# Performance work log

Measured on AMD Instinct MI355X. Metric: run time of the kernel, lower is better.

The kernel has to match this reference:

```python
import jax, jax.numpy as jnp
import numpy as np

N_U = 200000
N_I = 100000
DIM = 128
N_E = 1500000
N_LAYERS = 2


def setup_inputs() -> dict:
    key = jax.random.key(0)
    k1, k2, k3, k4 = jax.random.split(key, 4)
    # xavier-uniform-ish init (bounded values); exact init scheme irrelevant for kernel correctness
    bound = float(np.sqrt(6.0 / (N_U + DIM)))
    u_emb = jax.random.uniform(k1, (N_U, DIM), jnp.float32, -bound, bound)
    bound_i = float(np.sqrt(6.0 / (N_I + DIM)))
    i_emb = jax.random.uniform(k2, (N_I, DIM), jnp.float32, -bound_i, bound_i)
    u_idx = jax.random.randint(k3, (N_E,), 0, N_U, dtype=jnp.int64 if jax.config.jax_enable_x64 else jnp.int32)
    i_idx = jax.random.randint(k4, (N_E,), 0, N_I, dtype=jnp.int64 if jax.config.jax_enable_x64 else jnp.int32)
    return {"u_emb": u_emb, "i_emb": i_emb, "u_idx": u_idx, "i_idx": i_idx}


def _prop(x, r, c, n):
    # symmetric-normalized gather-scale-scatter (SpMM), as in _LightGCN._prop
    deg = jnp.bincount(jnp.concatenate([r, c]), length=n).astype(x.dtype)
    norm = (jnp.clip(deg[r], 1e-10) ** -0.5) * (jnp.clip(deg[c], 1e-10) ** -0.5)  # [2E]
    msg = x[c] * norm[:, None]  # [2E, dim]
    return jax.ops.segment_sum(msg, r, num_segments=n)


def reference(u_emb, i_emb, u_idx, i_idx):
    n_u = u_emb.shape[0]
    n = n_u + i_emb.shape[0]
    it = i_idx + n_u
    r = jnp.concatenate([u_idx, it])  # row (destination) indices
    c = jnp.concatenate([it, u_idx])  # col (source) indices
    x = jnp.concatenate([u_emb, i_emb], axis=0)  # [n, dim]
    outs = [x]
    for _ in range(N_LAYERS):
        x = _prop(x, r, c, n)
        outs.append(x)
    fin = jnp.mean(jnp.stack(outs), axis=0)
    return (fin[:n_u], fin[n_u:])
```

## Files before the change

kernel.cpp:

```cpp
#include <hip/hip_runtime.h>

#define DIM 128
#define NBLK 256
#define BKT_BITS 9
#define BKT_ROWS 512
#define MAXBUK 1024

using f16 = _Float16;
using f16x4 = __attribute__((ext_vector_type(4))) f16;
using f32x4 = __attribute__((ext_vector_type(4))) float;


__device__ __forceinline__ int permb(int b) { return ((b & 7) << 5) | (b >> 3); }

__global__ __launch_bounds__(256) void k_hist(const int* __restrict__ u_idx,
                                              const int* __restrict__ i_idx,
                                              int E, int n_u, int NBUK,
                                              int* __restrict__ hist) {
    __shared__ int h[MAXBUK];
    int b = blockIdx.x, tid = threadIdx.x;
    for (int j = tid; j < NBUK; j += 256) h[j] = 0;
    __syncthreads();
    int chunk = (E + NBLK - 1) / NBLK;
    int i0 = b * chunk, i1 = E < i0 + chunk ? E : i0 + chunk;
    for (int i = i0 + tid; i < i1; i += 256) {
        int u = __builtin_nontemporal_load(&u_idx[i]);
        int t = __builtin_nontemporal_load(&i_idx[i]) + n_u;
        atomicAdd(&h[u >> BKT_BITS], 1);
        atomicAdd(&h[t >> BKT_BITS], 1);
    }
    __syncthreads();
    int pb = permb(b);
    for (int j = tid; j < NBUK; j += 256) hist[j * NBLK + pb] = h[j];
}

__global__ __launch_bounds__(256) void k_scanB(int* __restrict__ hist,
                                               int* __restrict__ bb) {
    __shared__ int sh[256];
    int k = blockIdx.x, t = threadIdx.x;
    int v = hist[k * NBLK + t];
    sh[t] = v;
    __syncthreads();
    for (int off = 1; off < 256; off <<= 1) {
        int tmp = (t >= off) ? sh[t - off] : 0;
        __syncthreads();
        sh[t] += tmp;
        __syncthreads();
    }
    hist[k * NBLK + t] = sh[t] - v;
    if (t == 255) bb[k] = sh[255];
}

__global__ __launch_bounds__(1024) void k_scanT(int* __restrict__ bb, int NBUK) {
    __shared__ int sh[1024];
    int t = threadIdx.x;
    int v = (t < NBUK) ? bb[t] : 0;
    sh[t] = v;
    __syncthreads();
    for (int off = 1; off < 1024; off <<= 1) {
        int tmp = (t >= off) ? sh[t - off] : 0;
        __syncthreads();
        sh[t] += tmp;
        __syncthreads();
    }
    if (t < NBUK) bb[t] = sh[t] - v;
    if (t == NBUK - 1) bb[NBUK] = sh[t];
}

__global__ __launch_bounds__(256) void k_scatter(const int* __restrict__ u_idx,
                                                 const int* __restrict__ i_idx,
                                                 int E, int n_u, int NBUK,
                                                 const int* __restrict__ hist,
                                                 const int* __restrict__ bb,
                                                 unsigned* __restrict__ pre) {
    __shared__ int boff[MAXBUK];
    __shared__ int cnt[MAXBUK];
    int b = blockIdx.x, tid = threadIdx.x;
    int pb = permb(b);
    for (int j = tid; j < NBUK; j += 256) {
        boff[j] = bb[j] + hist[j * NBLK + pb];
        cnt[j] = 0;
    }
    __syncthreads();
    int chunk = (E + NBLK - 1) / NBLK;
    int i0 = b * chunk, i1 = E < i0 + chunk ? E : i0 + chunk;
    for (int i = i0 + tid; i < i1; i += 256) {
        int u = __builtin_nontemporal_load(&u_idx[i]);
        int t = __builtin_nontemporal_load(&i_idx[i]) + n_u;
        int ku = u >> BKT_BITS, kt = t >> BKT_BITS;
        int p1 = atomicAdd(&cnt[ku], 1);
        pre[boff[ku] + p1] = ((unsigned)t << BKT_BITS) | (unsigned)(u & (BKT_ROWS - 1));
        int p2 = atomicAdd(&cnt[kt], 1);
        pre[boff[kt] + p2] = ((unsigned)u << BKT_BITS) | (unsigned)(t & (BKT_ROWS - 1));
    }
}

__global__ __launch_bounds__(256) void k_place(const int* __restrict__ bb, int n, int n_u,
                                               const unsigned* __restrict__ pre,
                                               const float* __restrict__ u_emb,
                                               const float* __restrict__ i_emb,
                                               int* __restrict__ row_ptr,
                                               float* __restrict__ rnorm,
                                               int* __restrict__ adj,
                                               f16* __restrict__ xh0) {
    __shared__ int cnt[BKT_ROWS];
    __shared__ int cur[BKT_ROWS];
    __shared__ int ps[256];
    int b = blockIdx.x, t = threadIdx.x;
    int r0 = b << BKT_BITS;
    int base = bb[b], end = bb[b + 1];
    cnt[t] = 0;
    cnt[t + 256] = 0;
    __syncthreads();
    for (int i = base + t; i < end; i += 256)
        atomicAdd(&cnt[pre[i] & (BKT_ROWS - 1)], 1);
    __syncthreads();
    int a0 = cnt[2 * t], a1 = cnt[2 * t + 1];
    int pv = a0 + a1;
    ps[t] = pv;
    __syncthreads();
    for (int off = 1; off < 256; off <<= 1) {
        int tmp = (t >= off) ? ps[t - off] : 0;
        __syncthreads();
        ps[t] += tmp;
        __syncthreads();
    }
    int ex = ps[t] - pv;
    int e0 = base + ex;
    int e1 = e0 + a0;
    cur[2 * t] = e0;
    cur[2 * t + 1] = e1;
    int rows = n - r0; if (rows > BKT_ROWS) rows = BKT_ROWS;
    if (2 * t < rows) {
        row_ptr[r0 + 2 * t] = e0;
        rnorm[r0 + 2 * t] = (a0 > 0) ? rsqrtf(2.0f * (float)a0) : 0.0f;
    }
    if (2 * t + 1 < rows) {
        row_ptr[r0 + 2 * t + 1] = e1;
        rnorm[r0 + 2 * t + 1] = (a1 > 0) ? rsqrtf(2.0f * (float)a1) : 0.0f;
    }
    if (t == 0 && r0 + BKT_ROWS >= n) row_ptr[n] = end;
    __syncthreads();
    for (int i = base + t; i < end; i += 256) {
        unsigned p = pre[i];
        int rl = (int)(p & (BKT_ROWS - 1));
        int c = (int)(p >> BKT_BITS);
        int pos = atomicAdd(&cur[rl], 1);
        adj[pos] = c;
    }
    for (int g = t; g < rows * 32; g += 256) {
        int vr = g >> 5;
        int lane = g & 31;
        int v = r0 + vr;
        int d = cnt[vr];
        float r = (d > 0) ? rsqrtf(2.0f * (float)d) : 0.0f;
        const float* src = (v < n_u) ? (u_emb + (size_t)v * DIM)
                                     : (i_emb + (size_t)(v - n_u) * DIM);
        f32x4 x = __builtin_nontemporal_load(
            reinterpret_cast<const f32x4*>(src + lane * 4));
        f16x4 o;
        o[0] = (f16)(x[0] * r);
        o[1] = (f16)(x[1] * r);
        o[2] = (f16)(x[2] * r);
        o[3] = (f16)(x[3] * r);
        *reinterpret_cast<f16x4*>(xh0 + (size_t)v * DIM + lane * 4) = o;
    }
}


template <int MODE>
__global__ __launch_bounds__(256) void k_spmm(const int* __restrict__ row_ptr,
                                              const int* __restrict__ adj,
                                              const float* __restrict__ rnorm,
                                              const f16* __restrict__ xh,
                                              const f16* __restrict__ xh0e,
                                              const float* __restrict__ u_emb,
                                              const float* __restrict__ i_emb,
                                              int n_u, int n,
                                              float* __restrict__ y,
                                              f16* __restrict__ yh) {
    int g = blockIdx.x * blockDim.x + threadIdx.x;
    int row = g >> 5;
    int lane = g & 31;
    if (row >= n) return;
    int s = row_ptr[row];
    int e = row_ptr[row + 1];
    float rnr = rnorm[row];
    f32x4 acc = {0.f, 0.f, 0.f, 0.f};
    const f16* xb = xh + lane * 4;
    int e1 = e - 1;
    for (int k = s; k < e; k += 4) {
        int k1 = k + 1, k2 = k + 2, k3 = k + 3;
        int c0 = adj[k];
        int c1 = adj[(k1 <= e1) ? k1 : e1];
        int c2 = adj[(k2 <= e1) ? k2 : e1];
        int c3 = adj[(k3 <= e1) ? k3 : e1];
        float w1 = (k1 < e) ? 1.f : 0.f;
        float w2 = (k2 < e) ? 1.f : 0.f;
        float w3 = (k3 < e) ? 1.f : 0.f;
        f16x4 v0 = *reinterpret_cast<const f16x4*>(xb + (size_t)c0 * DIM);
        f16x4 v1 = *reinterpret_cast<const f16x4*>(xb + (size_t)c1 * DIM);
        f16x4 v2 = *reinterpret_cast<const f16x4*>(xb + (size_t)c2 * DIM);
        f16x4 v3 = *reinterpret_cast<const f16x4*>(xb + (size_t)c3 * DIM);
        acc[0] += (float)v0[0];
        acc[1] += (float)v0[1];
        acc[2] += (float)v0[2];
        acc[3] += (float)v0[3];
        acc[0] = fmaf((float)v1[0], w1, acc[0]);
        acc[1] = fmaf((float)v1[1], w1, acc[1]);
        acc[2] = fmaf((float)v1[2], w1, acc[2]);
        acc[3] = fmaf((float)v1[3], w1, acc[3]);
        acc[0] = fmaf((float)v2[0], w2, acc[0]);
        acc[1] = fmaf((float)v2[1], w2, acc[1]);
        acc[2] = fmaf((float)v2[2], w2, acc[2]);
        acc[3] = fmaf((float)v2[3], w2, acc[3]);
        acc[0] = fmaf((float)v3[0], w3, acc[0]);
        acc[1] = fmaf((float)v3[1], w3, acc[1]);
        acc[2] = fmaf((float)v3[2], w3, acc[2]);
        acc[3] = fmaf((float)v3[3], w3, acc[3]);
    }
    if (MODE == 0) {
        float sc = rnr * rnr;
        f16x4 h;
        h[0] = (f16)(acc[0] * sc);
        h[1] = (f16)(acc[1] * sc);
        h[2] = (f16)(acc[2] * sc);
        h[3] = (f16)(acc[3] * sc);
        *reinterpret_cast<f16x4*>(yh + (size_t)row * DIM + lane * 4) = h;
    } else {
        const float third = 1.0f / 3.0f;
        f32x4 o;
        if (rnr > 0.f) {
            f16x4 a0v = *reinterpret_cast<const f16x4*>(xh0e + (size_t)row * DIM + lane * 4);
            f16x4 a1v = *reinterpret_cast<const f16x4*>(xh + (size_t)row * DIM + lane * 4);
            float inv = 1.0f / rnr;
            o[0] = (((float)a0v[0] + (float)a1v[0]) * inv + acc[0] * rnr) * third;
            o[1] = (((float)a0v[1] + (float)a1v[1]) * inv + acc[1] * rnr) * third;
            o[2] = (((float)a0v[2] + (float)a1v[2]) * inv + acc[2] * rnr) * third;
            o[3] = (((float)a0v[3] + (float)a1v[3]) * inv + acc[3] * rnr) * third;
        } else {
            const float* x0b = (row < n_u) ? (u_emb + (size_t)row * DIM)
                                           : (i_emb + (size_t)(row - n_u) * DIM);
            f32x4 x0 = *reinterpret_cast<const f32x4*>(x0b + lane * 4);
            o[0] = x0[0] * third;
            o[1] = x0[1] * third;
            o[2] = x0[2] * third;
            o[3] = x0[3] * third;
        }
        __builtin_nontemporal_store(
            o, reinterpret_cast<f32x4*>(y + (size_t)row * DIM + lane * 4));
    }
}


extern "C" void kernel_launch(void* const* d_in, const int* in_sizes, int n_in,
                              void* d_out, int out_size, void* d_ws, size_t ws_size,
                              hipStream_t stream) {
    const float* u_emb = (const float*)d_in[0];
    const float* i_emb = (const float*)d_in[1];
    const int* u_idx = (const int*)d_in[2];
    const int* i_idx = (const int*)d_in[3];

    const int n_u = in_sizes[0] / DIM;
    const int n_i = in_sizes[1] / DIM;
    const int n = n_u + n_i;
    const int E = in_sizes[2];
    const int twoE = 2 * E;
    const int NBUK = (n + BKT_ROWS - 1) >> BKT_BITS;

    char* w = (char*)d_ws;
    auto alloc = [&](size_t bytes) -> void* {
        void* p = (void*)w;
        w += (bytes + 255) & ~(size_t)255;
        return p;
    };
    f16*   xh0     = (f16*)alloc((size_t)n * DIM * sizeof(f16));
    f16*   xh1     = (f16*)alloc((size_t)n * DIM * sizeof(f16));
    float* rnorm   = (float*)alloc((size_t)n * sizeof(float));
    int*   row_ptr = (int*)alloc((size_t)(n + 1) * sizeof(int));
    int*   adj     = (int*)alloc((size_t)twoE * sizeof(int));
    int*   hist    = (int*)alloc((size_t)NBUK * NBLK * sizeof(int));
    int*   bb      = (int*)alloc((size_t)(NBUK + 1) * sizeof(int));
    unsigned* pre  = (unsigned*)xh1;
    (void)ws_size;

    k_hist<<<NBLK, 256, 0, stream>>>(u_idx, i_idx, E, n_u, NBUK, hist);
    k_scanB<<<NBUK, 256, 0, stream>>>(hist, bb);
    k_scanT<<<1, 1024, 0, stream>>>(bb, NBUK);
    k_scatter<<<NBLK, 256, 0, stream>>>(u_idx, i_idx, E, n_u, NBUK, hist, bb, pre);
    k_place<<<NBUK, 256, 0, stream>>>(bb, n, n_u, pre, u_emb, i_emb,
                                      row_ptr, rnorm, adj, xh0);

    int sblocks = (int)(((long long)n * 32 + 255) / 256);
    k_spmm<0><<<sblocks, 256, 0, stream>>>(row_ptr, adj, rnorm, xh0, nullptr,
                                           nullptr, nullptr, n_u, n, nullptr, xh1);
    k_spmm<1><<<sblocks, 256, 0, stream>>>(row_ptr, adj, rnorm, xh1, xh0,
                                           u_emb, i_emb, n_u, n, (float*)d_out, nullptr);
}
```

Before: 384.5 us.

## Store gathered embeddings as scaled FP8 and carry a partial layer sum

The pre-scaled embedding tables read by both SpMM gathers are now stored in FP8 (e4m3 via packed convert intrinsics) with a fixed power-of-two scale instead of FP16, which halves the bytes per random row gather. The first SpMM pass also writes an FP16 partial sum of the input and layer-1 output, so the final pass reads one precomputed buffer instead of recombining two. This lowers gather bandwidth but adds precision loss from FP8 quantization, which could threaten tolerance, and the first pass now also reads the fp32 input embeddings.

After: 324.9 us. 15.5% less time.

```diff
diff --git a/kernel.cpp b/kernel.cpp
--- a/kernel.cpp
+++ b/kernel.cpp
@@ -6,9 +6,13 @@
 #define BKT_ROWS 512
 #define MAXBUK 1024
 
+#define S8   4096.0f
+#define INV8 (1.0f / 4096.0f)
+
 using f16 = _Float16;
 using f16x4 = __attribute__((ext_vector_type(4))) f16;
 using f32x4 = __attribute__((ext_vector_type(4))) float;
+using f32x2 = __attribute__((ext_vector_type(2))) float;
 
 
 __device__ __forceinline__ int permb(int b) { return ((b & 7) << 5) | (b >> 3); }
@@ -102,7 +106,7 @@
                                                int* __restrict__ row_ptr,
                                                float* __restrict__ rnorm,
                                                int* __restrict__ adj,
-                                               f16* __restrict__ xh0) {
+                                               unsigned* __restrict__ xq0) {
     __shared__ int cnt[BKT_ROWS];
     __shared__ int cur[BKT_ROWS];
     __shared__ int ps[256];
@@ -154,16 +158,14 @@
         int v = r0 + vr;
         int d = cnt[vr];
         float r = (d > 0) ? rsqrtf(2.0f * (float)d) : 0.0f;
+        float sr = r * S8;
         const float* src = (v < n_u) ? (u_emb + (size_t)v * DIM)
                                      : (i_emb + (size_t)(v - n_u) * DIM);
         f32x4 x = __builtin_nontemporal_load(
             reinterpret_cast<const f32x4*>(src + lane * 4));
-        f16x4 o;
-        o[0] = (f16)(x[0] * r);
-        o[1] = (f16)(x[1] * r);
-        o[2] = (f16)(x[2] * r);
-        o[3] = (f16)(x[3] * r);
-        *reinterpret_cast<f16x4*>(xh0 + (size_t)v * DIM + lane * 4) = o;
+        int q = __builtin_amdgcn_cvt_pk_fp8_f32(x[0] * sr, x[1] * sr, 0, false);
+        q = __builtin_amdgcn_cvt_pk_fp8_f32(x[2] * sr, x[3] * sr, q, true);
+        xq0[(size_t)v * 32 + lane] = (unsigned)q;
     }
 }
 
@@ -172,13 +174,14 @@
 __global__ __launch_bounds__(256) void k_spmm(const int* __restrict__ row_ptr,
                                               const int* __restrict__ adj,
                                               const float* __restrict__ rnorm,
-                                              const f16* __restrict__ xh,
-                                              const f16* __restrict__ xh0e,
+                                              const unsigned* __restrict__ xq,
+                                              const f16* __restrict__ p01,
                                               const float* __restrict__ u_emb,
                                               const float* __restrict__ i_emb,
                                               int n_u, int n,
                                               float* __restrict__ y,
-                                              f16* __restrict__ yh) {
+                                              unsigned* __restrict__ xq1o,
+                                              f16* __restrict__ p01o) {
     int g = blockIdx.x * blockDim.x + threadIdx.x;
     int row = g >> 5;
     int lane = g & 31;
@@ -187,7 +190,7 @@
     int e = row_ptr[row + 1];
     float rnr = rnorm[row];
     f32x4 acc = {0.f, 0.f, 0.f, 0.f};
-    const f16* xb = xh + lane * 4;
+    const unsigned* xb = xq + lane;
     int e1 = e - 1;
     for (int k = s; k < e; k += 4) {
         int k1 = k + 1, k2 = k + 2, k3 = k + 3;
@@ -198,55 +201,52 @@
         float w1 = (k1 < e) ? 1.f : 0.f;
         float w2 = (k2 < e) ? 1.f : 0.f;
         float w3 = (k3 < e) ? 1.f : 0.f;
-        f16x4 v0 = *reinterpret_cast<const f16x4*>(xb + (size_t)c0 * DIM);
-        f16x4 v1 = *reinterpret_cast<const f16x4*>(xb + (size_t)c1 * DIM);
-        f16x4 v2 = *reinterpret_cast<const f16x4*>(xb + (size_t)c2 * DIM);
-        f16x4 v3 = *reinterpret_cast<const f16x4*>(xb + (size_t)c3 * DIM);
-        acc[0] += (float)v0[0];
-        acc[1] += (float)v0[1];
-        acc[2] += (float)v0[2];
-        acc[3] += (float)v0[3];
-        acc[0] = fmaf((float)v1[0], w1, acc[0]);
-        acc[1] = fmaf((float)v1[1], w1, acc[1]);
-        acc[2] = fmaf((float)v1[2], w1, acc[2]);
-        acc[3] = fmaf((float)v1[3], w1, acc[3]);
-        acc[0] = fmaf((float)v2[0], w2, acc[0]);
-        acc[1] = fmaf((float)v2[1], w2, acc[1]);
-        acc[2] = fmaf((float)v2[2], w2, acc[2]);
-        acc[3] = fmaf((float)v2[3], w2, acc[3]);
-        acc[0] = fmaf((float)v3[0], w3, acc[0]);
-        acc[1] = fmaf((float)v3[1], w3, acc[1]);
-        acc[2] = fmaf((float)v3[2], w3, acc[2]);
-        acc[3] = fmaf((float)v3[3], w3, acc[3]);
+        unsigned q0 = xb[(size_t)c0 * 32];
+        unsigned q1 = xb[(size_t)c1 * 32];
+        unsigned q2 = xb[(size_t)c2 * 32];
+        unsigned q3 = xb[(size_t)c3 * 32];
+        f32x2 a0 = __builtin_amdgcn_cvt_pk_f32_fp8((int)q0, false);
+        f32x2 b0 = __builtin_amdgcn_cvt_pk_f32_fp8((int)q0, true);
+        acc[0] += a0[0]; acc[1] += a0[1]; acc[2] += b0[0]; acc[3] += b0[1];
+        f32x2 a1 = __builtin_amdgcn_cvt_pk_f32_fp8((int)q1, false);
+        f32x2 b1 = __builtin_amdgcn_cvt_pk_f32_fp8((int)q1, true);
+        acc[0] = fmaf(a1[0], w1, acc[0]); acc[1] = fmaf(a1[1], w1, acc[1]);
+        acc[2] = fmaf(b1[0], w1, acc[2]); acc[3] = fmaf(b1[1], w1, acc[3]);
+        f32x2 a2 = __builtin_amdgcn_cvt_pk_f32_fp8((int)q2, false);
+        f32x2 b2 = __builtin_amdgcn_cvt_pk_f32_fp8((int)q2, true);
+        acc[0] = fmaf(a2[0], w2, acc[0]); acc[1] = fmaf(a2[1], w2, acc[1]);
+        acc[2] = fmaf(b2[0], w2, acc[2]); acc[3] = fmaf(b2[1], w2, acc[3]);
+        f32x2 a3 = __builtin_amdgcn_cvt_pk_f32_fp8((int)q3, false);
+        f32x2 b3 = __builtin_amdgcn_cvt_pk_f32_fp8((int)q3, true);
+        acc[0] = fmaf(a3[0], w3, acc[0]); acc[1] = fmaf(a3[1], w3, acc[1]);
+        acc[2] = fmaf(b3[0], w3, acc[2]); acc[3] = fmaf(b3[1], w3, acc[3]);
     }
     if (MODE == 0) {
         float sc = rnr * rnr;
-        f16x4 h;
-        h[0] = (f16)(acc[0] * sc);
-        h[1] = (f16)(acc[1] * sc);
-        h[2] = (f16)(acc[2] * sc);
-        h[3] = (f16)(acc[3] * sc);
-        *reinterpret_cast<f16x4*>(yh + (size_t)row * DIM + lane * 4) = h;
+        int q = __builtin_amdgcn_cvt_pk_fp8_f32(acc[0] * sc, acc[1] * sc, 0, false);
+        q = __builtin_amdgcn_cvt_pk_fp8_f32(acc[2] * sc, acc[3] * sc, q, true);
+        xq1o[(size_t)row * 32 + lane] = (unsigned)q;
+        const float* x0b = (row < n_u) ? (u_emb + (size_t)row * DIM)
+                                       : (i_emb + (size_t)(row - n_u) * DIM);
+        f32x4 x0 = __builtin_nontemporal_load(
+            reinterpret_cast<const f32x4*>(x0b + lane * 4));
+        float t1 = rnr * INV8;
+        f16x4 p;
+        p[0] = (f16)(x0[0] + acc[0] * t1);
+        p[1] = (f16)(x0[1] + acc[1] * t1);
+        p[2] = (f16)(x0[2] + acc[2] * t1);
+        p[3] = (f16)(x0[3] + acc[3] * t1);
+        *reinterpret_cast<f16x4*>(p01o + (size_t)row * DIM + lane * 4) = p;
     } else {
+        f16x4 p = __builtin_nontemporal_load(
+            reinterpret_cast<const f16x4*>(p01 + (size_t)row * DIM + lane * 4));
         const float third = 1.0f / 3.0f;
+        float t2 = rnr * INV8;
         f32x4 o;
-        if (rnr > 0.f) {
-            f16x4 a0v = *reinterpret_cast<const f16x4*>(xh0e + (size_t)row * DIM + lane * 4);
-            f16x4 a1v = *reinterpret_cast<const f16x4*>(xh + (size_t)row * DIM + lane * 4);
-            float inv = 1.0f / rnr;
-            o[0] = (((float)a0v[0] + (float)a1v[0]) * inv + acc[0] * rnr) * third;
-            o[1] = (((float)a0v[1] + (float)a1v[1]) * inv + acc[1] * rnr) * third;
-            o[2] = (((float)a0v[2] + (float)a1v[2]) * inv + acc[2] * rnr) * third;
-            o[3] = (((float)a0v[3] + (float)a1v[3]) * inv + acc[3] * rnr) * third;
-        } else {
-            const float* x0b = (row < n_u) ? (u_emb + (size_t)row * DIM)
-                                           : (i_emb + (size_t)(row - n_u) * DIM);
-            f32x4 x0 = *reinterpret_cast<const f32x4*>(x0b + lane * 4);
-            o[0] = x0[0] * third;
-            o[1] = x0[1] * third;
-            o[2] = x0[2] * third;
-            o[3] = x0[3] * third;
-        }
+        o[0] = ((float)p[0] + acc[0] * t2) * third;
+        o[1] = ((float)p[1] + acc[1] * t2) * third;
+        o[2] = ((float)p[2] + acc[2] * t2) * third;
+        o[3] = ((float)p[3] + acc[3] * t2) * third;
         __builtin_nontemporal_store(
             o, reinterpret_cast<f32x4*>(y + (size_t)row * DIM + lane * 4));
     }
@@ -274,14 +274,15 @@
         w += (bytes + 255) & ~(size_t)255;
         return p;
     };
-    f16*   xh0     = (f16*)alloc((size_t)n * DIM * sizeof(f16));
-    f16*   xh1     = (f16*)alloc((size_t)n * DIM * sizeof(f16));
+    unsigned* xq0   = (unsigned*)alloc((size_t)n * 32 * sizeof(unsigned));
+    unsigned* xq1   = (unsigned*)alloc((size_t)n * 32 * sizeof(unsigned));
+    f16*   p01     = (f16*)alloc((size_t)n * DIM * sizeof(f16));
     float* rnorm   = (float*)alloc((size_t)n * sizeof(float));
     int*   row_ptr = (int*)alloc((size_t)(n + 1) * sizeof(int));
     int*   adj     = (int*)alloc((size_t)twoE * sizeof(int));
     int*   hist    = (int*)alloc((size_t)NBUK * NBLK * sizeof(int));
     int*   bb      = (int*)alloc((size_t)(NBUK + 1) * sizeof(int));
-    unsigned* pre  = (unsigned*)xh1;
+    unsigned* pre  = (unsigned*)p01;
     (void)ws_size;
 
     k_hist<<<NBLK, 256, 0, stream>>>(u_idx, i_idx, E, n_u, NBUK, hist);
@@ -289,11 +290,13 @@
     k_scanT<<<1, 1024, 0, stream>>>(bb, NBUK);
     k_scatter<<<NBLK, 256, 0, stream>>>(u_idx, i_idx, E, n_u, NBUK, hist, bb, pre);
     k_place<<<NBUK, 256, 0, stream>>>(bb, n, n_u, pre, u_emb, i_emb,
-                                      row_ptr, rnorm, adj, xh0);
+                                      row_ptr, rnorm, adj, xq0);
 
     int sblocks = (int)(((long long)n * 32 + 255) / 256);
-    k_spmm<0><<<sblocks, 256, 0, stream>>>(row_ptr, adj, rnorm, xh0, nullptr,
-                                           nullptr, nullptr, n_u, n, nullptr, xh1);
-    k_spmm<1><<<sblocks, 256, 0, stream>>>(row_ptr, adj, rnorm, xh1, xh0,
-                                           u_emb, i_emb, n_u, n, (float*)d_out, nullptr);
-}
+    k_spmm<0><<<sblocks, 256, 0, stream>>>(row_ptr, adj, rnorm, xq0, nullptr,
+                                           u_emb, i_emb, n_u, n,
+                                           nullptr, xq1, p01);
+    k_spmm<1><<<sblocks, 256, 0, stream>>>(row_ptr, adj, rnorm, xq1, p01,
+                                           nullptr, nullptr, n_u, n,
+                                           (float*)d_out, nullptr, nullptr);
+}
```
